# Kernel tuning notes

Hardware: AMD Instinct MI355X
Metric: run time of the kernel (lower is better)

The kernel has to match this reference:

```python
import jax, jax.numpy as jnp
import numpy as np

B, C, T, H, W = 32, 512, 16, 14, 14
DS = 7
HW = H * W
STD = 0.03


def setup_inputs() -> dict:
    key = jax.random.key(0)
    ks = jax.random.split(key, 6)
    x_in = jax.random.normal(ks[0], (B, C, T, HW), jnp.float32)
    # nn.Linear weights stored as (in, out) so forward is x @ W + b
    W1 = jax.random.truncated_normal(ks[1], -2.0, 2.0, (DS * DS * C, C), jnp.float32) * STD
    b1 = jnp.zeros((C,), jnp.float32)
    W2 = jax.random.truncated_normal(ks[2], -2.0, 2.0, (C, C // 8), jnp.float32) * STD
    b2 = jnp.zeros((C // 8,), jnp.float32)
    Wa = jax.random.truncated_normal(ks[3], -2.0, 2.0, (T * T, T // 2), jnp.float32) * STD
    Wd = jax.random.truncated_normal(ks[4], -2.0, 2.0, (T * T, T // 2), jnp.float32) * STD
    return {"x_in": x_in, "W1": W1, "b1": b1, "W2": W2, "b2": b2, "Wa": Wa, "Wd": Wd}


def _temporal_sample(x_in, idx):
    # Faithful to F.grid_sample(bilinear, padding_mode='border', align_corners=False)
    # on a (b, hw*c, t, 1) tensor: the width axis is size 1 and the grid x-coord is 0,
    # which maps exactly to pixel 0 with full weight, so only the t-axis matters.
    # normalize_grid uses n-1 = t-1; unnormalize (align_corners=False) gives:
    #   pixel = ((norm + 1) * t - 1) / 2 = idx * t / (t - 1) - 0.5
    b, c, t, hw = x_in.shape
    p = idx * (t / (t - 1)) - 0.5            # (b, t//2)
    i0 = jnp.floor(p)
    w = (p - i0)[:, None, :, None]           # (b, 1, t//2, 1)
    i0i = i0.astype(jnp.int32)
    i0c = jnp.clip(i0i, 0, t - 1)[:, None, :, None]
    i1c = jnp.clip(i0i + 1, 0, t - 1)[:, None, :, None]
    g0 = jnp.take_along_axis(x_in, jnp.broadcast_to(i0c, (b, c, t // 2, hw)), axis=2)
    g1 = jnp.take_along_axis(x_in, jnp.broadcast_to(i1c, (b, c, t // 2, hw)), axis=2)
    return (1.0 - w) * g0 + w * g1           # (b, c, t//2, hw)


def reference(x_in, W1, b1, W2, b2, Wa, Wd):
    b, c, t, hw = x_in.shape
    # (b, c, t, hw) -> (b, t, c, H, W)
    xi = x_in.reshape(b, c, t, H, W).transpose(0, 2, 1, 3, 4)
    # adaptive_avg_pool2d 14x14 -> 7x7 is an exact 2x2 mean
    xi = xi.reshape(b, t, c, DS, 2, DS, 2).mean(axis=(4, 6))      # (b, t, c, 7, 7)
    xi = xi.transpose(0, 1, 3, 4, 2).reshape(b, t, DS * DS * c)    # (b, t, 25088)
    h = jax.nn.gelu(xi @ W1 + b1, approximate=False)
    feat = h @ W2 + b2                                             # (b, t, c//8)
    scaler = 1.0 / c
    attn = jax.nn.softmax(scaler * jnp.einsum('btd,bsd->bts', feat, feat), axis=-1)
    flat = attn.reshape(b, t * t)
    receptive_field = 2.0
    off_a = jnp.tanh(flat @ Wa) * receptive_field                  # (b, t//2)
    off_d = jnp.tanh(flat @ Wd) * receptive_field
    idx_a = jnp.arange(0, t, 2, dtype=x_in.dtype)[None, :] + off_a
    idx_d = jnp.arange(1, t, 2, dtype=x_in.dtype)[None, :] + off_d
    x_a = _temporal_sample(x_in, idx_a)
    x_d = _temporal_sample(x_in, idx_d)
    return x_a, x_d
```

## Files before the change

### kernel.cpp

```cpp
#include <hip/hip_runtime.h>
#include <math.h>

#define CC 512
#define K1 25088
#define N1 512
#define NE 25690112

typedef unsigned short ushort_t;
typedef __attribute__((ext_vector_type(8))) short bf16x8;
typedef __attribute__((ext_vector_type(4))) float f32x4;
typedef __attribute__((address_space(3))) void* as3_void;
typedef const __attribute__((address_space(1))) void* as1_cvoid;

struct us4 { ushort_t a, b, c, d; };

__device__ __forceinline__ ushort_t f2bf(float f) {
  union { float f; unsigned u; } v; v.f = f;
  unsigned r = v.u + 0x7fffu + ((v.u >> 16) & 1u);
  return (ushort_t)(r >> 16);
}

__global__ __launch_bounds__(256)
void k_w1t(const float* __restrict__ W1, ushort_t* __restrict__ W1t) {
  __shared__ float tile[64][65];
  int k0 = blockIdx.x * 64;
  int n0 = blockIdx.y * 64;
  int tid = threadIdx.x;
  int rg = tid >> 4;
  int m  = tid & 15;
  for (int it = 0; it < 4; ++it) {
    int row = rg + it * 16;
    float4 v = *(const float4*)&W1[(size_t)(k0 + row) * N1 + n0 + m * 4];
    tile[row][m * 4 + 0] = v.x;
    tile[row][m * 4 + 1] = v.y;
    tile[row][m * 4 + 2] = v.z;
    tile[row][m * 4 + 3] = v.w;
  }
  __syncthreads();
  for (int it = 0; it < 4; ++it) {
    int n = rg + it * 16;
    int kb = m * 4;
    us4 o;
    o.a = f2bf(tile[kb + 0][n]);
    o.b = f2bf(tile[kb + 1][n]);
    o.c = f2bf(tile[kb + 2][n]);
    o.d = f2bf(tile[kb + 3][n]);
    *(us4*)&W1t[(size_t)(n0 + n) * K1 + k0 + kb] = o;
  }
}

__global__ __launch_bounds__(256)
void k_pool(const float* __restrict__ x, ushort_t* __restrict__ A) {
  __shared__ float s[64][197];
  int bx = blockIdx.x;
  int cch = bx & 7;
  int t = (bx >> 3) & 15;
  int b = bx >> 7;
  int c0 = cch * 64;
  int tid = threadIdx.x;
  for (int idx = tid; idx < 3136; idx += 256) {
    int c = idx / 49;
    int q = idx - c * 49;
    float4 v = *(const float4*)&x[(((size_t)(b * 512 + c0 + c) * 16) + t) * 196 + q * 4];
    s[c][q * 4 + 0] = v.x;
    s[c][q * 4 + 1] = v.y;
    s[c][q * 4 + 2] = v.z;
    s[c][q * 4 + 3] = v.w;
  }
  __syncthreads();
  ushort_t* dst = A + (size_t)(b * 16 + t) * K1 + c0;
  for (int o = tid; o < 3136; o += 256) {
    int ij = o >> 6;
    int c = o & 63;
    int i = ij / 7;
    int j = ij - i * 7;
    int pos = i * 28 + j * 2;
    float v = (s[c][pos] + s[c][pos + 1] + s[c][pos + 14] + s[c][pos + 15]) * 0.25f;
    dst[ij * 512 + c] = f2bf(v);
  }
}

__global__ __launch_bounds__(256)
void k_gemm1(const ushort_t* __restrict__ A, const ushort_t* __restrict__ Bt,
             float* __restrict__ Cp) {
  __shared__ __align__(16) short As[4][128][8];
  __shared__ __align__(16) short Bs[4][128][8];
  int row0 = blockIdx.x * 128;
  int col0 = blockIdx.y * 128;
  int k0 = blockIdx.z * 512;
  int lane = threadIdx.x & 63;
  int wave = threadIdx.x >> 6;
  int wm = (wave & 1) * 64;
  int wn = (wave >> 1) * 64;
  f32x4 acc[4][4] = {};

  for (int kk = 0; kk < 512; kk += 32) {
    __syncthreads();
    for (int t = 0; t < 2; ++t) {
      int wt = wave * 2 + t;
      int ch = wt >> 1;
      int r0 = (wt & 1) * 64;
      int rr = r0 + lane;
      const ushort_t* ga = A  + (size_t)(row0 + rr) * K1 + (k0 + kk + ch * 8);
      const ushort_t* gb = Bt + (size_t)(col0 + rr) * K1 + (k0 + kk + ch * 8);
      __builtin_amdgcn_global_load_lds((as1_cvoid)ga, (as3_void)&As[ch][r0][0], 16, 0, 0);
      __builtin_amdgcn_global_load_lds((as1_cvoid)gb, (as3_void)&Bs[ch][r0][0], 16, 0, 0);
    }
    __syncthreads();
    int ml = lane & 15, q = lane >> 4;
    bf16x8 af[4], bfr[4];
    for (int sm = 0; sm < 4; ++sm)
      af[sm] = *(const bf16x8*)&As[q][wm + sm * 16 + ml][0];
    for (int sn = 0; sn < 4; ++sn)
      bfr[sn] = *(const bf16x8*)&Bs[q][wn + sn * 16 + ml][0];
    for (int sm = 0; sm < 4; ++sm)
      for (int sn = 0; sn < 4; ++sn)
        acc[sm][sn] = __builtin_amdgcn_mfma_f32_16x16x32_bf16(af[sm], bfr[sn], acc[sm][sn], 0, 0, 0);
  }
  int ml = lane & 15, q = lane >> 4;
  float* out = Cp + (size_t)blockIdx.z * 262144;
  for (int sm = 0; sm < 4; ++sm)
    for (int sn = 0; sn < 4; ++sn)
      for (int rg = 0; rg < 4; ++rg) {
        int row = row0 + wm + sm * 16 + q * 4 + rg;
        int col = col0 + wn + sn * 16 + ml;
        out[row * N1 + col] = acc[sm][sn][rg];
      }
}

__global__ __launch_bounds__(256)
void k_reduce(const float* __restrict__ Cp, const float* __restrict__ b1,
              float* __restrict__ h) {
  int i = blockIdx.x * 256 + threadIdx.x;
  float a = 0.f;
  for (int z = 0; z < 49; ++z) a += Cp[(size_t)z * 262144 + i];
  float xv = a + b1[i & 511];
  h[i] = 0.5f * xv * (1.0f + erff(xv * 0.70710678118654752f));
}

__global__ __launch_bounds__(256)
void k_head(const float* __restrict__ h, const float* __restrict__ W2,
            const float* __restrict__ b2, const float* __restrict__ Wa,
            const float* __restrict__ Wd, float* __restrict__ offs) {
  int b = blockIdx.x;
  __shared__ float hs[16][512];
  __shared__ float fl[16][65];
  __shared__ float lg[256];
  int tid = threadIdx.x;
  for (int idx = tid; idx < 8192; idx += 256)
    hs[idx >> 9][idx & 511] = h[(size_t)b * 8192 + idx];
  __syncthreads();
  {
    int n = tid & 63;
    int tg = tid >> 6;
    float acc0 = b2[n], acc1 = acc0, acc2 = acc0, acc3 = acc0;
    for (int k = 0; k < 512; ++k) {
      float w = W2[k * 64 + n];
      acc0 += hs[tg][k] * w;
      acc1 += hs[tg + 4][k] * w;
      acc2 += hs[tg + 8][k] * w;
      acc3 += hs[tg + 12][k] * w;
    }
    fl[tg][n] = acc0;
    fl[tg + 4][n] = acc1;
    fl[tg + 8][n] = acc2;
    fl[tg + 12][n] = acc3;
  }
  __syncthreads();
  {
    int t = tid >> 4, s = tid & 15;
    float a = 0.f;
    for (int d = 0; d < 64; ++d) a += fl[t][d] * fl[s][d];
    lg[tid] = a * (1.0f / 512.0f);
  }
  __syncthreads();
  if (tid < 16) {
    float m = -1e30f;
    for (int s = 0; s < 16; ++s) m = fmaxf(m, lg[tid * 16 + s]);
    float e[16], sum = 0.f;
    for (int s = 0; s < 16; ++s) { e[s] = expf(lg[tid * 16 + s] - m); sum += e[s]; }
    float inv = 1.0f / sum;
    for (int s = 0; s < 16; ++s) lg[tid * 16 + s] = e[s] * inv;
  }
  __syncthreads();
  if (tid < 16) {
    int which = tid >> 3, col = tid & 7;
    const float* W = which ? Wd : Wa;
    float a = 0.f;
    for (int f = 0; f < 256; ++f) a += lg[f] * W[f * 8 + col];
    offs[b * 16 + tid] = tanhf(a) * 2.0f;
  }
}

__global__ __launch_bounds__(256)
void k_sample(const float* __restrict__ x, const float* __restrict__ offs,
              float* __restrict__ out) {
  int bc = blockIdx.x;
  int b = bc >> 9;
  __shared__ float4 xs[16 * 49];
  __shared__ int i0s[16], i1s[16];
  __shared__ float wfr[16];
  int tid = threadIdx.x;
  const float4* src = (const float4*)(x + (size_t)bc * 16 * 196);
  for (int i = tid; i < 784; i += 256) xs[i] = src[i];
  if (tid < 16) {
    int which = tid >> 3, to = tid & 7;
    float idx = (float)(2 * to + which) + offs[b * 16 + tid];
    float p = idx * (16.0f / 15.0f) - 0.5f;
    float fl = floorf(p);
    int i0 = (int)fl;
    wfr[tid] = p - fl;
    i0s[tid] = min(max(i0, 0), 15);
    i1s[tid] = min(max(i0 + 1, 0), 15);
  }
  __syncthreads();
  float4* out4 = (float4*)out;
  for (int oi = tid; oi < 784; oi += 256) {
    int which = oi / 392;
    int rem = oi - which * 392;
    int to = rem / 49;
    int q = rem - to * 49;
    int slot = which * 8 + to;
    float w = wfr[slot];
    float4 g0 = xs[i0s[slot] * 49 + q];
    float4 g1 = xs[i1s[slot] * 49 + q];
    float4 o;
    o.x = g0.x + w * (g1.x - g0.x);
    o.y = g0.y + w * (g1.y - g0.y);
    o.z = g0.z + w * (g1.z - g0.z);
    o.w = g0.w + w * (g1.w - g0.w);
    out4[(size_t)which * (NE / 4) + (size_t)(bc * 8 + to) * 49 + q] = o;
  }
}

extern "C" void kernel_launch(void* const* d_in, const int* in_sizes, int n_in,
                              void* d_out, int out_size, void* d_ws, size_t ws_size,
                              hipStream_t stream) {
  const float* x  = (const float*)d_in[0];
  const float* W1 = (const float*)d_in[1];
  const float* b1 = (const float*)d_in[2];
  const float* W2 = (const float*)d_in[3];
  const float* b2 = (const float*)d_in[4];
  const float* Wa = (const float*)d_in[5];
  const float* Wd = (const float*)d_in[6];
  float* out = (float*)d_out;

  char* w = (char*)d_ws;
  ushort_t* Abf  = (ushort_t*)(w);
  ushort_t* W1t  = (ushort_t*)(w + 25690112);
  float*    Cp   = (float*)(w + 51380224);
  float*    h    = (float*)(w + 51380224 + 51380224);
  float*    feat_offs = (float*)(w + 51380224 + 51380224 + 1048576);

  float* offs = feat_offs;

  k_w1t<<<dim3(392, 8), 256, 0, stream>>>(W1, W1t);
  k_pool<<<4096, 256, 0, stream>>>(x, Abf);
  k_gemm1<<<dim3(4, 4, 49), 256, 0, stream>>>(Abf, W1t, Cp);
  k_reduce<<<1024, 256, 0, stream>>>(Cp, b1, h);
  k_head<<<32, 256, 0, stream>>>(h, W2, b2, Wa, Wd, offs);
  k_sample<<<16384, 256, 0, stream>>>(x, offs, out);
}
```

Before: 547.1 us.

## Merge weight transpose and pooling into one launch; vectorize reduce; parallelize head

Combines the W1 transpose/bf16 conversion and the activation pooling into one kernel that dispatches on block index, removing a launch and letting both independent stages overlap on the device. The split-K reduction now uses float4 loads with a quarter of the blocks. The head kernel moves to 512 threads, replaces the serial softmax with shuffle reductions, and splits the offset projection across 256 threads with a partial-sum table. Shared memory per block for the merged kernel is sized to the larger pooling buffer, which may reduce occupancy for the transpose blocks.

```diff
diff --git a/kernel.cpp b/kernel.cpp
--- a/kernel.cpp
+++ b/kernel.cpp
@@ -20,63 +20,68 @@
   return (ushort_t)(r >> 16);
 }
 
-__global__ __launch_bounds__(256)
-void k_w1t(const float* __restrict__ W1, ushort_t* __restrict__ W1t) {
-  __shared__ float tile[64][65];
-  int k0 = blockIdx.x * 64;
-  int n0 = blockIdx.y * 64;
+__device__ __forceinline__ float gelu(float x) {
+  return 0.5f * x * (1.0f + erff(x * 0.70710678118654752f));
+}
+
+__global__ __launch_bounds__(256)
+void k_stage(const float* __restrict__ x, const float* __restrict__ W1,
+             ushort_t* __restrict__ A, ushort_t* __restrict__ W1t) {
+  __shared__ __align__(16) float smem[64 * 197];
   int tid = threadIdx.x;
-  int rg = tid >> 4;
-  int m  = tid & 15;
-  for (int it = 0; it < 4; ++it) {
-    int row = rg + it * 16;
-    float4 v = *(const float4*)&W1[(size_t)(k0 + row) * N1 + n0 + m * 4];
-    tile[row][m * 4 + 0] = v.x;
-    tile[row][m * 4 + 1] = v.y;
-    tile[row][m * 4 + 2] = v.z;
-    tile[row][m * 4 + 3] = v.w;
-  }
-  __syncthreads();
-  for (int it = 0; it < 4; ++it) {
-    int n = rg + it * 16;
-    int kb = m * 4;
-    us4 o;
-    o.a = f2bf(tile[kb + 0][n]);
-    o.b = f2bf(tile[kb + 1][n]);
-    o.c = f2bf(tile[kb + 2][n]);
-    o.d = f2bf(tile[kb + 3][n]);
-    *(us4*)&W1t[(size_t)(n0 + n) * K1 + k0 + kb] = o;
-  }
-}
-
-__global__ __launch_bounds__(256)
-void k_pool(const float* __restrict__ x, ushort_t* __restrict__ A) {
-  __shared__ float s[64][197];
-  int bx = blockIdx.x;
-  int cch = bx & 7;
-  int t = (bx >> 3) & 15;
-  int b = bx >> 7;
-  int c0 = cch * 64;
-  int tid = threadIdx.x;
-  for (int idx = tid; idx < 3136; idx += 256) {
-    int c = idx / 49;
-    int q = idx - c * 49;
-    float4 v = *(const float4*)&x[(((size_t)(b * 512 + c0 + c) * 16) + t) * 196 + q * 4];
-    s[c][q * 4 + 0] = v.x;
-    s[c][q * 4 + 1] = v.y;
-    s[c][q * 4 + 2] = v.z;
-    s[c][q * 4 + 3] = v.w;
-  }
-  __syncthreads();
-  ushort_t* dst = A + (size_t)(b * 16 + t) * K1 + c0;
-  for (int o = tid; o < 3136; o += 256) {
-    int ij = o >> 6;
-    int c = o & 63;
-    int i = ij / 7;
-    int j = ij - i * 7;
-    int pos = i * 28 + j * 2;
-    float v = (s[c][pos] + s[c][pos + 1] + s[c][pos + 14] + s[c][pos + 15]) * 0.25f;
-    dst[ij * 512 + c] = f2bf(v);
+  if (blockIdx.x < 3136) {
+    float (*tile)[65] = (float (*)[65])smem;
+    int u = blockIdx.x;
+    int k0 = (u % 392) * 64;
+    int n0 = (u / 392) * 64;
+    int rg = tid >> 4;
+    int m  = tid & 15;
+    for (int it = 0; it < 4; ++it) {
+      int row = rg + it * 16;
+      float4 v = *(const float4*)&W1[(size_t)(k0 + row) * N1 + n0 + m * 4];
+      tile[row][m * 4 + 0] = v.x;
+      tile[row][m * 4 + 1] = v.y;
+      tile[row][m * 4 + 2] = v.z;
+      tile[row][m * 4 + 3] = v.w;
+    }
+    __syncthreads();
+    for (int it = 0; it < 4; ++it) {
+      int n = rg + it * 16;
+      int kb = m * 4;
+      us4 o;
+      o.a = f2bf(tile[kb + 0][n]);
+      o.b = f2bf(tile[kb + 1][n]);
+      o.c = f2bf(tile[kb + 2][n]);
+      o.d = f2bf(tile[kb + 3][n]);
+      *(us4*)&W1t[(size_t)(n0 + n) * K1 + k0 + kb] = o;
+    }
+  } else {
+    float (*s)[197] = (float (*)[197])smem;
+    int bx = blockIdx.x - 3136;
+    int cch = bx & 7;
+    int t = (bx >> 3) & 15;
+    int b = bx >> 7;
+    int c0 = cch * 64;
+    for (int idx = tid; idx < 3136; idx += 256) {
+      int c = idx / 49;
+      int q = idx - c * 49;
+      float4 v = *(const float4*)&x[(((size_t)(b * 512 + c0 + c) * 16) + t) * 196 + q * 4];
+      s[c][q * 4 + 0] = v.x;
+      s[c][q * 4 + 1] = v.y;
+      s[c][q * 4 + 2] = v.z;
+      s[c][q * 4 + 3] = v.w;
+    }
+    __syncthreads();
+    ushort_t* dst = A + (size_t)(b * 16 + t) * K1 + c0;
+    for (int o = tid; o < 3136; o += 256) {
+      int ij = o >> 6;
+      int c = o & 63;
+      int i = ij / 7;
+      int j = ij - i * 7;
+      int pos = i * 28 + j * 2;
+      float v = (s[c][pos] + s[c][pos + 1] + s[c][pos + 14] + s[c][pos + 15]) * 0.25f;
+      dst[ij * 512 + c] = f2bf(v);
+    }
   }
 }
 
@@ -131,14 +136,23 @@
 __global__ __launch_bounds__(256)
 void k_reduce(const float* __restrict__ Cp, const float* __restrict__ b1,
               float* __restrict__ h) {
-  int i = blockIdx.x * 256 + threadIdx.x;
-  float a = 0.f;
-  for (int z = 0; z < 49; ++z) a += Cp[(size_t)z * 262144 + i];
-  float xv = a + b1[i & 511];
-  h[i] = 0.5f * xv * (1.0f + erff(xv * 0.70710678118654752f));
-}
-
-__global__ __launch_bounds__(256)
+  int i4 = blockIdx.x * 256 + threadIdx.x;
+  const float4* cp4 = (const float4*)Cp;
+  float4 a = cp4[i4];
+  for (int z = 1; z < 49; ++z) {
+    float4 v = cp4[(size_t)z * 65536 + i4];
+    a.x += v.x; a.y += v.y; a.z += v.z; a.w += v.w;
+  }
+  float4 bb = ((const float4*)b1)[i4 & 127];
+  float4 r;
+  r.x = gelu(a.x + bb.x);
+  r.y = gelu(a.y + bb.y);
+  r.z = gelu(a.z + bb.z);
+  r.w = gelu(a.w + bb.w);
+  ((float4*)h)[i4] = r;
+}
+
+__global__ __launch_bounds__(512)
 void k_head(const float* __restrict__ h, const float* __restrict__ W2,
             const float* __restrict__ b2, const float* __restrict__ Wa,
             const float* __restrict__ Wd, float* __restrict__ offs) {
@@ -146,48 +160,56 @@
   __shared__ float hs[16][512];
   __shared__ float fl[16][65];
   __shared__ float lg[256];
+  __shared__ float pr[16][17];
   int tid = threadIdx.x;
-  for (int idx = tid; idx < 8192; idx += 256)
-    hs[idx >> 9][idx & 511] = h[(size_t)b * 8192 + idx];
+  {
+    const float4* src = (const float4*)(h + (size_t)b * 8192);
+    float4* dst = (float4*)&hs[0][0];
+    for (int i = tid; i < 2048; i += 512) dst[i] = src[i];
+  }
   __syncthreads();
   {
     int n = tid & 63;
     int tg = tid >> 6;
-    float acc0 = b2[n], acc1 = acc0, acc2 = acc0, acc3 = acc0;
+    float acc0 = 0.f, acc1 = 0.f;
+    #pragma unroll 4
     for (int k = 0; k < 512; ++k) {
       float w = W2[k * 64 + n];
       acc0 += hs[tg][k] * w;
-      acc1 += hs[tg + 4][k] * w;
-      acc2 += hs[tg + 8][k] * w;
-      acc3 += hs[tg + 12][k] * w;
-    }
-    fl[tg][n] = acc0;
-    fl[tg + 4][n] = acc1;
-    fl[tg + 8][n] = acc2;
-    fl[tg + 12][n] = acc3;
-  }
-  __syncthreads();
-  {
+      acc1 += hs[tg + 8][k] * w;
+    }
+    float bias = b2[n];
+    fl[tg][n] = acc0 + bias;
+    fl[tg + 8][n] = acc1 + bias;
+  }
+  __syncthreads();
+  if (tid < 256) {
     int t = tid >> 4, s = tid & 15;
     float a = 0.f;
     for (int d = 0; d < 64; ++d) a += fl[t][d] * fl[s][d];
-    lg[tid] = a * (1.0f / 512.0f);
+    a *= (1.0f / 512.0f);
+    float m = a;
+    for (int w = 1; w < 16; w <<= 1) m = fmaxf(m, __shfl_xor(m, w, 16));
+    float e = expf(a - m);
+    float sum = e;
+    for (int w = 1; w < 16; w <<= 1) sum += __shfl_xor(sum, w, 16);
+    lg[tid] = e / sum;
+  }
+  __syncthreads();
+  if (tid < 256) {
+    int o = tid & 15;
+    int ch = tid >> 4;
+    const float* W = (o >= 8) ? Wd : Wa;
+    int col = o & 7;
+    float a = 0.f;
+    int f0 = ch * 16;
+    for (int f = f0; f < f0 + 16; ++f) a += lg[f] * W[f * 8 + col];
+    pr[ch][o] = a;
   }
   __syncthreads();
   if (tid < 16) {
-    float m = -1e30f;
-    for (int s = 0; s < 16; ++s) m = fmaxf(m, lg[tid * 16 + s]);
-    float e[16], sum = 0.f;
-    for (int s = 0; s < 16; ++s) { e[s] = expf(lg[tid * 16 + s] - m); sum += e[s]; }
-    float inv = 1.0f / sum;
-    for (int s = 0; s < 16; ++s) lg[tid * 16 + s] = e[s] * inv;
-  }
-  __syncthreads();
-  if (tid < 16) {
-    int which = tid >> 3, col = tid & 7;
-    const float* W = which ? Wd : Wa;
     float a = 0.f;
-    for (int f = 0; f < 256; ++f) a += lg[f] * W[f * 8 + col];
+    for (int ch = 0; ch < 16; ++ch) a += pr[ch][tid];
     offs[b * 16 + tid] = tanhf(a) * 2.0f;
   }
 }
@@ -250,14 +272,11 @@
   ushort_t* W1t  = (ushort_t*)(w + 25690112);
   float*    Cp   = (float*)(w + 51380224);
   float*    h    = (float*)(w + 51380224 + 51380224);
-  float*    feat_offs = (float*)(w + 51380224 + 51380224 + 1048576);
-
-  float* offs = feat_offs;
-
-  k_w1t<<<dim3(392, 8), 256, 0, stream>>>(W1, W1t);
-  k_pool<<<4096, 256, 0, stream>>>(x, Abf);
+  float*    offs = (float*)(w + 51380224 + 51380224 + 1048576);
+
+  k_stage<<<7232, 256, 0, stream>>>(x, W1, Abf, W1t);
   k_gemm1<<<dim3(4, 4, 49), 256, 0, stream>>>(Abf, W1t, Cp);
-  k_reduce<<<1024, 256, 0, stream>>>(Cp, b1, h);
-  k_head<<<32, 256, 0, stream>>>(h, W2, b2, Wa, Wd, offs);
+  k_reduce<<<256, 256, 0, stream>>>(Cp, b1, h);
+  k_head<<<32, 512, 0, stream>>>(h, W2, b2, Wa, Wd, offs);
   k_sample<<<16384, 256, 0, stream>>>(x, offs, out);
 }
```

After: 551.2 us. Within noise of the previous version (+0.7%).
